# Performance work log

Hardware: AMD Instinct MI355X
Metric: run time of the kernel (lower is better)

Reference implementation:

```python
import jax, jax.numpy as jnp
import numpy as np

DIM = 512
HEADS = 8


def setup_inputs() -> dict:
    key = jax.random.key(0)
    k1, k2, k3 = jax.random.split(key, 3)
    x = jax.random.normal(k1, (4, DIM, 64, 64), dtype=jnp.float32)
    # kaiming_normal fan_out, linear: std = 1/sqrt(fan_out)
    w_qkv = jax.random.normal(k2, (3 * DIM, DIM), dtype=jnp.float32) / np.sqrt(3 * DIM)
    b_qkv = jnp.zeros((3 * DIM,), dtype=jnp.float32)
    w_proj = jax.random.normal(k3, (DIM, DIM), dtype=jnp.float32) / np.sqrt(DIM)
    b_proj = jnp.zeros((DIM,), dtype=jnp.float32)
    return {"x": x, "w_qkv": w_qkv, "b_qkv": b_qkv, "w_proj": w_proj, "b_proj": b_proj}


def reference(x, w_qkv, b_qkv, w_proj, b_proj):
    B, C, H, W = x.shape
    N = H * W
    hd = C // HEADS
    scale = hd ** -0.5
    x_flat = x.reshape(B, C, N).transpose(0, 2, 1)          # [B, N, C]
    qkv = x_flat @ w_qkv.T + b_qkv                           # [B, N, 3C]
    q, k, v = jnp.split(qkv, 3, axis=-1)
    q = q.reshape(B, N, HEADS, hd).transpose(0, 2, 1, 3)     # [B, h, N, d]
    k = k.reshape(B, N, HEADS, hd).transpose(0, 2, 1, 3)
    v = v.reshape(B, N, HEADS, hd).transpose(0, 2, 1, 3)
    attn = jnp.einsum('bhnd,bhmd->bhnm', q, k) * scale       # [B, h, N, N]
    attn = jnp.clip(attn, -10.0, 10.0)
    attn = jax.nn.softmax(attn, axis=-1)
    out = jnp.einsum('bhnm,bhmd->bhnd', attn, v)             # [B, h, N, d]
    out = out.transpose(0, 2, 1, 3).reshape(B, N, C)         # [B, N, C]
    out = out @ w_proj.T + b_proj
    out = out.transpose(0, 2, 1).reshape(B, C, H, W)
    return x + out
```

## Files before the change

### kernel.cpp

```cpp
#include <hip/hip_runtime.h>

typedef float f32x4 __attribute__((ext_vector_type(4)));
typedef __bf16 bf16x8 __attribute__((ext_vector_type(8)));
typedef unsigned short u16;
typedef unsigned int u32;
typedef u16 u16x4 __attribute__((ext_vector_type(4)));
typedef u16 u16x8 __attribute__((ext_vector_type(8)));

#define DEV static __device__ __forceinline__

constexpr int B = 4, C = 512, NH = 8, HD = 64, NN = 4096, C3 = 1536;
constexpr float K_PRESCALE = 0.125f * 1.4426950408889634f;
constexpr float CLIP2 = 10.0f * 1.4426950408889634f;

DEV u16 f2bf(float f) { union { __bf16 b; u16 s; } u; u.b = (__bf16)f; return u.s; }

#if __has_builtin(__builtin_amdgcn_exp2f)
DEV float fast_exp2(float x) { return __builtin_amdgcn_exp2f(x); }
#else
DEV float fast_exp2(float x) { return __expf(x * 0.6931471805599453f); }
#endif

#if __has_builtin(__builtin_amdgcn_fmed3f)
DEV float clamp2(float x) { return __builtin_amdgcn_fmed3f(x, -CLIP2, CLIP2); }
#else
DEV float clamp2(float x) { return fminf(fmaxf(x, -CLIP2), CLIP2); }
#endif

#if __has_builtin(__builtin_amdgcn_global_load_lds)
#define HAVE_GLL 1
DEV void gll16(const void* g, void* l) {
  __builtin_amdgcn_global_load_lds(
      (const __attribute__((address_space(1))) void*)g,
      (__attribute__((address_space(3))) void*)l, 16, 0, 0);
}
#else
#define HAVE_GLL 0
#endif

__global__ __launch_bounds__(256) void k_transpose(const float* __restrict__ x,
                                                   u16* __restrict__ Xt) {
  __shared__ float tile[64][65];
  const int n0 = blockIdx.x * 64, c0 = blockIdx.y * 64, b = blockIdx.z;
  const int t = threadIdx.x;
  const int cl = t >> 4, n4 = (t & 15) * 4;
#pragma unroll
  for (int rep = 0; rep < 4; ++rep) {
    const int c = rep * 16 + cl;
    const f32x4 v = *(const f32x4*)(x + ((size_t)(b * C + c0 + c)) * NN + n0 + n4);
#pragma unroll
    for (int j = 0; j < 4; ++j) tile[c][n4 + j] = v[j];
  }
  __syncthreads();
#pragma unroll
  for (int rep = 0; rep < 16; ++rep) {
    const int n = rep * 4 + (t >> 6);
    const int c = t & 63;
    Xt[((size_t)(b * NN + n0 + n)) * C + c0 + c] = f2bf(tile[c][n]);
  }
}

__global__ __launch_bounds__(256) void k_cvtw(const float* __restrict__ wq,
                                              const float* __restrict__ wp,
                                              u16* __restrict__ Wq, u16* __restrict__ Wp) {
  const int idx = blockIdx.x * 256 + threadIdx.x;
  const int NQ = C3 * C / 4;
  const float* src;
  u16* dst;
  int i4;
  if (idx < NQ) { src = wq; dst = Wq; i4 = idx; }
  else          { src = wp; dst = Wp; i4 = idx - NQ; }
  const f32x4 v = *(const f32x4*)(src + (size_t)i4 * 4);
  u16x4 o;
#pragma unroll
  for (int j = 0; j < 4; ++j) o[j] = f2bf(v[j]);
  *(u16x4*)(dst + (size_t)i4 * 4) = o;
}

__global__ __launch_bounds__(256) void k_qkv(const u16* __restrict__ Xt,
                                             const u16* __restrict__ W,
                                             const float* __restrict__ bias,
                                             u16* __restrict__ Q, u16* __restrict__ Kq,
                                             u16* __restrict__ Vt) {
  __shared__ u16 smem[16384];
  u16* Alds = smem;
  u16* Blds = smem + 8192;
  const int nt = blockIdx.x, mt = blockIdx.y, b = blockIdx.z;
  const int t = threadIdx.x, w = t >> 6, l = t & 63;
  const int l15 = l & 15, l4 = l >> 4;
  const int wr = w >> 1, wc = w & 1;
  f32x4 acc[4][4] = {};
  const u16* Abase = Xt + (size_t)(b * NN + nt * 128) * C;
  const u16* Bbase = W + (size_t)(mt * 128) * C;

  for (int kt = 0; kt < C / 64; ++kt) {
    __syncthreads();
#if HAVE_GLL
#pragma unroll
    for (int i = 0; i < 4; ++i) {
      const int cch = t + 256 * i;
      const int r = cch >> 3;
      const int sc = ((cch & 7) * 16) ^ ((r & 7) << 4);
      gll16((const char*)(Abase + (size_t)r * C + kt * 64) + sc, (char*)Alds + cch * 16);
      gll16((const char*)(Bbase + (size_t)r * C + kt * 64) + sc, (char*)Blds + cch * 16);
    }
#else
#pragma unroll
    for (int i = 0; i < 4; ++i) {
      const int cch = t + 256 * i;
      const int r = cch >> 3, kb = (cch & 7) * 16;
      const int sw = kb ^ ((r & 7) << 4);
      *(f32x4*)((char*)Alds + r * 128 + sw) =
          *(const f32x4*)((const char*)(Abase + (size_t)r * C + kt * 64) + kb);
      *(f32x4*)((char*)Blds + r * 128 + sw) =
          *(const f32x4*)((const char*)(Bbase + (size_t)r * C + kt * 64) + kb);
    }
#endif
    __syncthreads();
#pragma unroll
    for (int ks = 0; ks < 2; ++ks) {
      bf16x8 af[4], bfr[4];
#pragma unroll
      for (int ri = 0; ri < 4; ++ri) {
        const int row = wr * 64 + ri * 16 + l15;
        af[ri] = *(const bf16x8*)((const char*)Alds + row * 128 +
                                  ((ks * 64 + l4 * 16) ^ ((row & 7) << 4)));
      }
#pragma unroll
      for (int cj = 0; cj < 4; ++cj) {
        const int row = wc * 64 + cj * 16 + l15;
        bfr[cj] = *(const bf16x8*)((const char*)Blds + row * 128 +
                                   ((ks * 64 + l4 * 16) ^ ((row & 7) << 4)));
      }
#pragma unroll
      for (int ri = 0; ri < 4; ++ri)
#pragma unroll
        for (int cj = 0; cj < 4; ++cj)
          acc[ri][cj] = __builtin_amdgcn_mfma_f32_16x16x32_bf16(af[ri], bfr[cj], acc[ri][cj], 0, 0, 0);
    }
  }

  __syncthreads();
  const int sec = mt >> 2;
  const int mtl = mt & 3;
  if (sec < 2) {
#pragma unroll
    for (int ri = 0; ri < 4; ++ri)
#pragma unroll
      for (int cj = 0; cj < 4; ++cj) {
        const int m_l = wc * 64 + cj * 16 + l15;
        const float bv = bias[mt * 128 + m_l];
        const float sc = (sec == 1) ? K_PRESCALE : 1.0f;
#pragma unroll
        for (int r = 0; r < 4; ++r) {
          const int n_l = wr * 64 + ri * 16 + l4 * 4 + r;
          *(u16*)((char*)smem + n_l * 256 + ((m_l * 2) ^ ((n_l & 7) << 4))) =
              f2bf((acc[ri][cj][r] + bv) * sc);
        }
      }
    __syncthreads();
    u16* dst = (sec == 0) ? Q : Kq;
#pragma unroll
    for (int rep = 0; rep < 8; ++rep) {
      const int idx = rep * 256 + t;
      const int n_l = idx >> 4, ch = idx & 15;
      const u16x8 v = *(const u16x8*)((char*)smem + n_l * 256 + ((ch * 16) ^ ((n_l & 7) << 4)));
      const int hh = mtl * 2 + (ch >> 3), dd = (ch & 7) * 8;
      *(u16x8*)(dst + ((size_t)(b * NH + hh) * NN + nt * 128 + n_l) * HD + dd) = v;
    }
  } else {
#pragma unroll
    for (int ri = 0; ri < 4; ++ri)
#pragma unroll
      for (int cj = 0; cj < 4; ++cj) {
        const int m_l = wc * 64 + cj * 16 + l15;
        const float bv = bias[mt * 128 + m_l];
        const int nb = wr * 64 + ri * 16 + l4 * 4;
        u16x4 pv;
#pragma unroll
        for (int r = 0; r < 4; ++r) pv[r] = f2bf(acc[ri][cj][r] + bv);
        *(u16x4*)((char*)smem + m_l * 256 + ((nb * 2) ^ ((m_l & 7) << 4))) = pv;
      }
    __syncthreads();
#pragma unroll
    for (int rep = 0; rep < 8; ++rep) {
      const int idx = rep * 256 + t;
      const int m_l = idx >> 4, ch = idx & 15;
      const u16x8 v = *(const u16x8*)((char*)smem + m_l * 256 + ((ch * 16) ^ ((m_l & 7) << 4)));
      const int hh = mtl * 2 + (m_l >> 6), dd = m_l & 63;
      *(u16x8*)(Vt + ((size_t)(b * NH + hh) * HD + dd) * NN + nt * 128 + ch * 8) = v;
    }
  }
}

__global__ __launch_bounds__(256) void k_attn(const u16* __restrict__ Q,
                                              const u16* __restrict__ K,
                                              const u16* __restrict__ Vt,
                                              u16* __restrict__ AO) {
  __shared__ u16 Klds[4096];
  __shared__ u16 Vlds[4096];
  __shared__ u16 Plds[4096];
  const int qt = blockIdx.x, h = blockIdx.y, b = blockIdx.z;
  const int bh = b * NH + h;
  const int t = threadIdx.x, w = t >> 6, l = t & 63;
  const int l15 = l & 15, l4 = l >> 4;
  const int q0 = qt * 64;

  const u16* qb = Q + ((size_t)bh * NN + q0 + w * 16 + l15) * HD + l4 * 8;
  bf16x8 qf[2];
  qf[0] = *(const bf16x8*)(qb);
  qf[1] = *(const bf16x8*)(qb + 32);

  union { u16 s; __bf16 b; } ob;
  ob.s = 0x3F80;
  bf16x8 ones;
#pragma unroll
  for (int j = 0; j < 8; ++j) ones[j] = ob.b;

  f32x4 o[4] = {};
  f32x4 rsa = {};

  const int sr = t >> 3, scb = (t & 7) * 16;
  const int ssw = scb ^ ((sr & 7) << 4);
  char* kwp = (char*)Klds + sr * 128 + ssw;
  char* vwp = (char*)Vlds + sr * 128 + ssw;
  const char* kg = (const char*)(K + (size_t)bh * NN * HD) + sr * 128 + scb;
  const char* vg = (const char*)(Vt + (size_t)bh * HD * NN) + (size_t)sr * 8192 + scb;

  const int sw7 = (l15 & 7) << 4;

  f32x4 kr0 = *(const f32x4*)kg;
  f32x4 kr1 = *(const f32x4*)(kg + 4096);
  f32x4 vr0 = *(const f32x4*)vg;
  f32x4 vr1 = *(const f32x4*)(vg + (size_t)32 * 8192);
  *(f32x4*)kwp = kr0;
  *(f32x4*)(kwp + 4096) = kr1;
  *(f32x4*)vwp = vr0;
  *(f32x4*)(vwp + 4096) = vr1;
  __syncthreads();

  constexpr int NT = NN / 64;
  for (int kv = 0; kv < NT; ++kv) {
    if (kv + 1 < NT) {
      kg += 8192;
      vg += 128;
      kr0 = *(const f32x4*)kg;
      kr1 = *(const f32x4*)(kg + 4096);
      vr0 = *(const f32x4*)vg;
      vr1 = *(const f32x4*)(vg + (size_t)32 * 8192);
    }

    f32x4 s[4] = {};
#pragma unroll
    for (int ks = 0; ks < 2; ++ks) {
#pragma unroll
      for (int cj = 0; cj < 4; ++cj) {
        const bf16x8 kf = *(const bf16x8*)((const char*)Klds + (cj * 16 + l15) * 128 +
                                           ((ks * 64 + l4 * 16) ^ sw7));
        s[cj] = __builtin_amdgcn_mfma_f32_16x16x32_bf16(qf[ks], kf, s[cj], 0, 0, 0);
      }
    }
#pragma unroll
    for (int cj = 0; cj < 4; ++cj) {
      const int colb = (cj * 16 + l15) * 2;
#pragma unroll
      for (int r = 0; r < 4; ++r) {
        const float p = fast_exp2(clamp2(s[cj][r]));
        const int row = w * 16 + l4 * 4 + r;
        *(u16*)((char*)Plds + row * 128 + (colb ^ ((row & 7) << 4))) = f2bf(p);
      }
    }

#pragma unroll
    for (int ks = 0; ks < 2; ++ks) {
      const int prow = w * 16 + l15;
      const bf16x8 pa = *(const bf16x8*)((const char*)Plds + prow * 128 +
                                         ((ks * 64 + l4 * 16) ^ sw7));
#pragma unroll
      for (int cj = 0; cj < 4; ++cj) {
        const bf16x8 vf = *(const bf16x8*)((const char*)Vlds + (cj * 16 + l15) * 128 +
                                           ((ks * 64 + l4 * 16) ^ sw7));
        o[cj] = __builtin_amdgcn_mfma_f32_16x16x32_bf16(pa, vf, o[cj], 0, 0, 0);
      }
      rsa = __builtin_amdgcn_mfma_f32_16x16x32_bf16(pa, ones, rsa, 0, 0, 0);
    }
    __syncthreads();

    if (kv + 1 < NT) {
      *(f32x4*)kwp = kr0;
      *(f32x4*)(kwp + 4096) = kr1;
      *(f32x4*)vwp = vr0;
      *(f32x4*)(vwp + 4096) = vr1;
    }
    __syncthreads();
  }

  float inv[4];
#pragma unroll
  for (int r = 0; r < 4; ++r) inv[r] = 1.0f / rsa[r];
#pragma unroll
  for (int cj = 0; cj < 4; ++cj)
#pragma unroll
    for (int r = 0; r < 4; ++r) {
      const int n = q0 + w * 16 + l4 * 4 + r;
      const int c = h * 64 + cj * 16 + l15;
      AO[((size_t)(b * NN + n)) * C + c] = f2bf(o[cj][r] * inv[r]);
    }
}

__global__ __launch_bounds__(256) void k_proj(const u16* __restrict__ AO,
                                              const u16* __restrict__ Wp,
                                              const float* __restrict__ bias,
                                              const float* __restrict__ x,
                                              float* __restrict__ out) {
  __shared__ u16 smem[16384];
  u16* Alds = smem;
  u16* Blds = smem + 8192;
  const int nt = blockIdx.x, ct = blockIdx.y, b = blockIdx.z;
  const int t = threadIdx.x, w = t >> 6, l = t & 63;
  const int l15 = l & 15, l4 = l >> 4;
  const int wr = w >> 1, wc = w & 1;
  f32x4 acc[4][4] = {};
  const u16* Abase = AO + (size_t)(b * NN + nt * 128) * C;
  const u16* Bbase = Wp + (size_t)(ct * 128) * C;

  for (int kt = 0; kt < C / 64; ++kt) {
    __syncthreads();
#if HAVE_GLL
#pragma unroll
    for (int i = 0; i < 4; ++i) {
      const int cch = t + 256 * i;
      const int r = cch >> 3;
      const int sc = ((cch & 7) * 16) ^ ((r & 7) << 4);
      gll16((const char*)(Abase + (size_t)r * C + kt * 64) + sc, (char*)Alds + cch * 16);
      gll16((const char*)(Bbase + (size_t)r * C + kt * 64) + sc, (char*)Blds + cch * 16);
    }
#else
#pragma unroll
    for (int i = 0; i < 4; ++i) {
      const int cch = t + 256 * i;
      const int r = cch >> 3, kb = (cch & 7) * 16;
      const int sw = kb ^ ((r & 7) << 4);
      *(f32x4*)((char*)Alds + r * 128 + sw) =
          *(const f32x4*)((const char*)(Abase + (size_t)r * C + kt * 64) + kb);
      *(f32x4*)((char*)Blds + r * 128 + sw) =
          *(const f32x4*)((const char*)(Bbase + (size_t)r * C + kt * 64) + kb);
    }
#endif
    __syncthreads();
#pragma unroll
    for (int ks = 0; ks < 2; ++ks) {
      bf16x8 af[4], bfr[4];
#pragma unroll
      for (int ri = 0; ri < 4; ++ri) {
        const int row = wr * 64 + ri * 16 + l15;
        af[ri] = *(const bf16x8*)((const char*)Alds + row * 128 +
                                  ((ks * 64 + l4 * 16) ^ ((row & 7) << 4)));
      }
#pragma unroll
      for (int cj = 0; cj < 4; ++cj) {
        const int row = wc * 64 + cj * 16 + l15;
        bfr[cj] = *(const bf16x8*)((const char*)Blds + row * 128 +
                                   ((ks * 64 + l4 * 16) ^ ((row & 7) << 4)));
      }
#pragma unroll
      for (int ri = 0; ri < 4; ++ri)
#pragma unroll
        for (int cj = 0; cj < 4; ++cj)
          acc[ri][cj] = __builtin_amdgcn_mfma_f32_16x16x32_bf16(af[ri], bfr[cj], acc[ri][cj], 0, 0, 0);
    }
  }

  float* fs = (float*)smem;
  __syncthreads();
#pragma unroll
  for (int p = 0; p < 2; ++p) {
    if (p) __syncthreads();
    if (wc == p) {
#pragma unroll
      for (int ri = 0; ri < 4; ++ri)
#pragma unroll
        for (int cj = 0; cj < 4; ++cj) {
          const int co = cj * 16 + l15;
          const float bv = bias[ct * 128 + p * 64 + co];
          const int nb = wr * 64 + ri * 16 + l4 * 4;
          f32x4 vv;
#pragma unroll
          for (int r = 0; r < 4; ++r) vv[r] = acc[ri][cj][r] + bv;
          *(f32x4*)((char*)fs + co * 512 + ((nb * 4) ^ ((co & 7) << 4))) = vv;
        }
    }
    __syncthreads();
#pragma unroll
    for (int rep = 0; rep < 8; ++rep) {
      const int idx = rep * 256 + t;
      const int co = idx >> 5, ch = idx & 31;
      f32x4 vv = *(const f32x4*)((char*)fs + co * 512 + ((ch * 16) ^ ((co & 7) << 4)));
      const size_t base = ((size_t)(b * C + ct * 128 + p * 64 + co)) * NN + nt * 128 + ch * 4;
      const f32x4 xr = *(const f32x4*)(x + base);
#pragma unroll
      for (int r = 0; r < 4; ++r) vv[r] += xr[r];
      *(f32x4*)(out + base) = vv;
    }
  }
}

extern "C" void kernel_launch(void* const* d_in, const int* in_sizes, int n_in,
                              void* d_out, int out_size, void* d_ws, size_t ws_size,
                              hipStream_t stream) {
  const float* x      = (const float*)d_in[0];
  const float* w_qkv  = (const float*)d_in[1];
  const float* b_qkv  = (const float*)d_in[2];
  const float* w_proj = (const float*)d_in[3];
  const float* b_proj = (const float*)d_in[4];
  float* out = (float*)d_out;
  char* ws = (char*)d_ws;

  const size_t SZ_XT = (size_t)B * NN * C * 2;
  const size_t SZ_WQ = (size_t)C3 * C * 2;
  const size_t SZ_WP = (size_t)C * C * 2;
  const size_t SZ_QK = (size_t)B * NH * NN * HD * 2;

  u16* Xt = (u16*)(ws);
  u16* Wq = (u16*)(ws + SZ_XT);
  u16* Wp = (u16*)(ws + SZ_XT + SZ_WQ);
  u16* Qb = (u16*)(ws + SZ_XT + SZ_WQ + SZ_WP);
  u16* Kb = (u16*)(ws + SZ_XT + SZ_WQ + SZ_WP + SZ_QK);
  u16* Vt = (u16*)(ws + SZ_XT + SZ_WQ + SZ_WP + 2 * SZ_QK);
  u16* AO = Xt;

  k_transpose<<<dim3(NN / 64, C / 64, B), 256, 0, stream>>>(x, Xt);
  k_cvtw<<<dim3((C3 * C + C * C) / 4 / 256), 256, 0, stream>>>(w_qkv, w_proj, Wq, Wp);
  k_qkv<<<dim3(NN / 128, C3 / 128, B), 256, 0, stream>>>(Xt, Wq, b_qkv, Qb, Kb, Vt);
  k_attn<<<dim3(NN / 64, NH, B), 256, 0, stream>>>(Qb, Kb, Vt, AO);
  k_proj<<<dim3(NN / 128, C / 128, B), 256, 0, stream>>>(AO, Wp, b_proj, x, out);
}
```

Baseline: 378.7 us.

## Process two key/value tiles per attention loop iteration with split prefetch streams

The attention kernel now stages two 64-key K/V tiles per loop iteration, one from the first half of the sequence and one from the second half, instead of one tile. This halves the number of block-wide barriers and LDS refill phases. It also doubles the global loads in flight per prefetch, which aims to hide memory latency better. In exchange it adds LDS (from 24 KB to 40 KB per block) and registers, while the launch bound now requests 4 blocks per CU, which may limit occupancy or force spills.

```diff
diff --git a/kernel.cpp b/kernel.cpp
--- a/kernel.cpp
+++ b/kernel.cpp
@@ -193,12 +193,14 @@
   }
 }
 
-__global__ __launch_bounds__(256) void k_attn(const u16* __restrict__ Q,
-                                              const u16* __restrict__ K,
-                                              const u16* __restrict__ Vt,
-                                              u16* __restrict__ AO) {
-  __shared__ u16 Klds[4096];
-  __shared__ u16 Vlds[4096];
+__global__ __launch_bounds__(256, 4) void k_attn(const u16* __restrict__ Q,
+                                                 const u16* __restrict__ K,
+                                                 const u16* __restrict__ Vt,
+                                                 u16* __restrict__ AO) {
+  __shared__ u16 KldsA[4096];
+  __shared__ u16 VldsA[4096];
+  __shared__ u16 KldsB[4096];
+  __shared__ u16 VldsB[4096];
   __shared__ u16 Plds[4096];
   const int qt = blockIdx.x, h = blockIdx.y, b = blockIdx.z;
   const int bh = b * NH + h;
@@ -221,76 +223,100 @@
   f32x4 rsa = {};
 
   const int sr = t >> 3, scb = (t & 7) * 16;
-  const int ssw = scb ^ ((sr & 7) << 4);
-  char* kwp = (char*)Klds + sr * 128 + ssw;
-  char* vwp = (char*)Vlds + sr * 128 + ssw;
-  const char* kg = (const char*)(K + (size_t)bh * NN * HD) + sr * 128 + scb;
-  const char* vg = (const char*)(Vt + (size_t)bh * HD * NN) + (size_t)sr * 8192 + scb;
+  const int so = sr * 128 + (scb ^ ((sr & 7) << 4));
+  const char* kgA = (const char*)(K + (size_t)bh * NN * HD) + sr * 128 + scb;
+  const char* vgA = (const char*)(Vt + (size_t)bh * HD * NN) + (size_t)sr * 8192 + scb;
+  const char* kgB = kgA + (size_t)32 * 8192;
+  const char* vgB = vgA + 32 * 128;
 
   const int sw7 = (l15 & 7) << 4;
 
-  f32x4 kr0 = *(const f32x4*)kg;
-  f32x4 kr1 = *(const f32x4*)(kg + 4096);
-  f32x4 vr0 = *(const f32x4*)vg;
-  f32x4 vr1 = *(const f32x4*)(vg + (size_t)32 * 8192);
-  *(f32x4*)kwp = kr0;
-  *(f32x4*)(kwp + 4096) = kr1;
-  *(f32x4*)vwp = vr0;
-  *(f32x4*)(vwp + 4096) = vr1;
+  {
+    const f32x4 a0 = *(const f32x4*)kgA;
+    const f32x4 a1 = *(const f32x4*)(kgA + 4096);
+    const f32x4 a2 = *(const f32x4*)vgA;
+    const f32x4 a3 = *(const f32x4*)(vgA + (size_t)32 * 8192);
+    const f32x4 b0 = *(const f32x4*)kgB;
+    const f32x4 b1 = *(const f32x4*)(kgB + 4096);
+    const f32x4 b2 = *(const f32x4*)vgB;
+    const f32x4 b3 = *(const f32x4*)(vgB + (size_t)32 * 8192);
+    *(f32x4*)((char*)KldsA + so) = a0;
+    *(f32x4*)((char*)KldsA + so + 4096) = a1;
+    *(f32x4*)((char*)VldsA + so) = a2;
+    *(f32x4*)((char*)VldsA + so + 4096) = a3;
+    *(f32x4*)((char*)KldsB + so) = b0;
+    *(f32x4*)((char*)KldsB + so + 4096) = b1;
+    *(f32x4*)((char*)VldsB + so) = b2;
+    *(f32x4*)((char*)VldsB + so + 4096) = b3;
+  }
   __syncthreads();
 
-  constexpr int NT = NN / 64;
-  for (int kv = 0; kv < NT; ++kv) {
-    if (kv + 1 < NT) {
-      kg += 8192;
-      vg += 128;
-      kr0 = *(const f32x4*)kg;
-      kr1 = *(const f32x4*)(kg + 4096);
-      vr0 = *(const f32x4*)vg;
-      vr1 = *(const f32x4*)(vg + (size_t)32 * 8192);
-    }
-
-    f32x4 s[4] = {};
-#pragma unroll
-    for (int ks = 0; ks < 2; ++ks) {
+  constexpr int NT2 = NN / 128;
+  f32x4 ka0, ka1, va0, va1, kb0, kb1, vb0, vb1;
+  for (int kv = 0; kv < NT2; ++kv) {
+    const bool more = (kv + 1 < NT2);
+    if (more) {
+      kgA += 8192; vgA += 128; kgB += 8192; vgB += 128;
+      ka0 = *(const f32x4*)kgA;
+      ka1 = *(const f32x4*)(kgA + 4096);
+      va0 = *(const f32x4*)vgA;
+      va1 = *(const f32x4*)(vgA + (size_t)32 * 8192);
+      kb0 = *(const f32x4*)kgB;
+      kb1 = *(const f32x4*)(kgB + 4096);
+      vb0 = *(const f32x4*)vgB;
+      vb1 = *(const f32x4*)(vgB + (size_t)32 * 8192);
+    }
+
+#pragma unroll
+    for (int st = 0; st < 2; ++st) {
+      const char* kbase = st ? (const char*)KldsB : (const char*)KldsA;
+      const char* vbase = st ? (const char*)VldsB : (const char*)VldsA;
+
+      f32x4 s[4] = {};
+#pragma unroll
+      for (int ks = 0; ks < 2; ++ks) {
+#pragma unroll
+        for (int cj = 0; cj < 4; ++cj) {
+          const bf16x8 kf = *(const bf16x8*)(kbase + (cj * 16 + l15) * 128 +
+                                             ((ks * 64 + l4 * 16) ^ sw7));
+          s[cj] = __builtin_amdgcn_mfma_f32_16x16x32_bf16(qf[ks], kf, s[cj], 0, 0, 0);
+        }
+      }
 #pragma unroll
       for (int cj = 0; cj < 4; ++cj) {
-        const bf16x8 kf = *(const bf16x8*)((const char*)Klds + (cj * 16 + l15) * 128 +
+        const int colb = (cj * 16 + l15) * 2;
+#pragma unroll
+        for (int r = 0; r < 4; ++r) {
+          const float p = fast_exp2(clamp2(s[cj][r]));
+          const int row = w * 16 + l4 * 4 + r;
+          *(u16*)((char*)Plds + row * 128 + (colb ^ ((row & 7) << 4))) = f2bf(p);
+        }
+      }
+#pragma unroll
+      for (int ks = 0; ks < 2; ++ks) {
+        const int prow = w * 16 + l15;
+        const bf16x8 pa = *(const bf16x8*)((const char*)Plds + prow * 128 +
                                            ((ks * 64 + l4 * 16) ^ sw7));
-        s[cj] = __builtin_amdgcn_mfma_f32_16x16x32_bf16(qf[ks], kf, s[cj], 0, 0, 0);
-      }
-    }
-#pragma unroll
-    for (int cj = 0; cj < 4; ++cj) {
-      const int colb = (cj * 16 + l15) * 2;
-#pragma unroll
-      for (int r = 0; r < 4; ++r) {
-        const float p = fast_exp2(clamp2(s[cj][r]));
-        const int row = w * 16 + l4 * 4 + r;
-        *(u16*)((char*)Plds + row * 128 + (colb ^ ((row & 7) << 4))) = f2bf(p);
-      }
-    }
-
-#pragma unroll
-    for (int ks = 0; ks < 2; ++ks) {
-      const int prow = w * 16 + l15;
-      const bf16x8 pa = *(const bf16x8*)((const char*)Plds + prow * 128 +
-                                         ((ks * 64 + l4 * 16) ^ sw7));
-#pragma unroll
-      for (int cj = 0; cj < 4; ++cj) {
-        const bf16x8 vf = *(const bf16x8*)((const char*)Vlds + (cj * 16 + l15) * 128 +
-                                           ((ks * 64 + l4 * 16) ^ sw7));
-        o[cj] = __builtin_amdgcn_mfma_f32_16x16x32_bf16(pa, vf, o[cj], 0, 0, 0);
-      }
-      rsa = __builtin_amdgcn_mfma_f32_16x16x32_bf16(pa, ones, rsa, 0, 0, 0);
-    }
-    __syncthreads();
-
-    if (kv + 1 < NT) {
-      *(f32x4*)kwp = kr0;
-      *(f32x4*)(kwp + 4096) = kr1;
-      *(f32x4*)vwp = vr0;
-      *(f32x4*)(vwp + 4096) = vr1;
+#pragma unroll
+        for (int cj = 0; cj < 4; ++cj) {
+          const bf16x8 vf = *(const bf16x8*)(vbase + (cj * 16 + l15) * 128 +
+                                             ((ks * 64 + l4 * 16) ^ sw7));
+          o[cj] = __builtin_amdgcn_mfma_f32_16x16x32_bf16(pa, vf, o[cj], 0, 0, 0);
+        }
+        rsa = __builtin_amdgcn_mfma_f32_16x16x32_bf16(pa, ones, rsa, 0, 0, 0);
+      }
+    }
+
+    __syncthreads();
+    if (more) {
+      *(f32x4*)((char*)KldsA + so) = ka0;
+      *(f32x4*)((char*)KldsA + so + 4096) = ka1;
+      *(f32x4*)((char*)VldsA + so) = va0;
+      *(f32x4*)((char*)VldsA + so + 4096) = va1;
+      *(f32x4*)((char*)KldsB + so) = kb0;
+      *(f32x4*)((char*)KldsB + so + 4096) = kb1;
+      *(f32x4*)((char*)VldsB + so) = vb0;
+      *(f32x4*)((char*)VldsB + so + 4096) = vb1;
     }
     __syncthreads();
   }
```

Measured after the change: 356.2 us. -5.9%, faster.
